# Kernel optimization log

Measured on AMD Instinct MI355X. Metric: run time of the kernel, lower is better.

The kernel has to match this reference:

```python
import jax, jax.numpy as jnp
import numpy as np

N = 50000
E = 800000
D_IN, D_HID, D_OUT = 128, 128, 64


def setup_inputs() -> dict:
    key = jax.random.key(0)
    ks = jax.random.split(key, 8)
    x = jax.random.normal(ks[0], (N, D_IN), dtype=jnp.float32)
    edge_index = jax.random.randint(ks[1], (2, E), 0, N, dtype=jnp.int64)
    # Glorot-ish init for GCNConv linear weights + zero bias (PyG default bias=True)
    def lin(k, din, dout):
        s = 1.0 / np.sqrt(din)
        return jax.random.uniform(k, (din, dout), jnp.float32, -s, s)
    return {
        "x": x,
        "edge_index": edge_index,
        "W1": lin(ks[2], D_IN, D_HID), "b1": jnp.zeros((D_HID,), jnp.float32),
        "W2": lin(ks[3], D_HID, D_HID), "b2": jnp.zeros((D_HID,), jnp.float32),
        "W3": lin(ks[4], D_HID, D_OUT), "b3": jnp.zeros((D_OUT,), jnp.float32),
    }


def _prep_edges(edge_index, n):
    # add self loops (PyG GCNConv default add_self_loops=True)
    loop = jnp.arange(n, dtype=edge_index.dtype)
    src = jnp.concatenate([edge_index[0], loop])
    dst = jnp.concatenate([edge_index[1], loop])
    deg = jax.ops.segment_sum(jnp.ones_like(dst, dtype=jnp.float32), dst, num_segments=n)
    dinv = jnp.where(deg > 0, jax.lax.rsqrt(deg), 0.0)
    norm = dinv[src] * dinv[dst]  # symmetric normalization per edge
    return src, dst, norm


def _gcn_conv(h, W, b, src, dst, norm, n):
    h = h @ W                                   # [N, dout]
    msg = h[src] * norm[:, None]                # [E+N, dout] gather
    out = jax.ops.segment_sum(msg, dst, num_segments=n)  # scatter-add
    return out + b


def reference(x, edge_index, W1, b1, W2, b2, W3, b3):
    src, dst, norm = _prep_edges(edge_index, N)
    h = jax.nn.relu(_gcn_conv(x, W1, b1, src, dst, norm, N))
    h = jax.nn.relu(_gcn_conv(h, W2, b2, src, dst, norm, N))
    return _gcn_conv(h, W3, b3, src, dst, norm, N)  # eval mode: dropout is identity
```

## Files before the change

kernel.cpp:

```cpp
#include <hip/hip_runtime.h>
#include <hip/hip_fp16.h>
#include <math.h>

#define NN 50000
#define NE 800000
#define RSTRIDE 104
#define RAWSTRIDE 96
#define NBUCK 196
#define BCAP 4608
#define ACH 4096

using bf8v = __attribute__((ext_vector_type(8))) short;
using f4v  = __attribute__((ext_vector_type(4))) float;

__device__ inline unsigned short f2bf(float f) {
    unsigned int u = __float_as_uint(f);
    u += 0x7FFFu + ((u >> 16) & 1u);
    return (unsigned short)(u >> 16);
}
__device__ inline float bflo(unsigned int d) { return __uint_as_float(d << 16); }
__device__ inline float bfhi(unsigned int d) { return __uint_as_float(d & 0xFFFF0000u); }
__device__ inline float ew(unsigned int u) {
    return __half2float(__ushort_as_half((unsigned short)(u >> 16)));
}
__device__ inline unsigned int epack(int col, float w) {
    return (unsigned int)col | ((unsigned int)__half_as_ushort(__float2half(w)) << 16);
}


__global__ __launch_bounds__(256) void bin_kernel(const int* __restrict__ src,
                                                  const int* __restrict__ dst,
                                                  int* __restrict__ gcursor,
                                                  unsigned int* __restrict__ bst) {
    __shared__ unsigned int items[ACH];
    __shared__ int cnt[256], pref[257], gstart[256];
    const int t = threadIdx.x;
    cnt[t] = 0;
    __syncthreads();
    const int base = blockIdx.x * ACH;

    unsigned int my[16]; int myb[16], myr[16];
    #pragma unroll
    for (int i = 0; i < 16; ++i) {
        int e = base + i * 256 + t;
        my[i] = 0; myb[i] = -1; myr[i] = 0;
        if (e < NE) {
            int d = dst[e], s = src[e];
            my[i] = (unsigned int)s | ((unsigned int)d << 16);
            int b = d >> 8;
            myb[i] = b;
            myr[i] = atomicAdd(&cnt[b], 1);
        }
    }
    __syncthreads();
    if (t == 0) {
        int run = 0;
        for (int b = 0; b < 256; ++b) { pref[b] = run; run += cnt[b]; }
        pref[256] = run;
    }
    __syncthreads();
    if (cnt[t] > 0) gstart[t] = atomicAdd(&gcursor[t], cnt[t]);
    __syncthreads();
    #pragma unroll
    for (int i = 0; i < 16; ++i)
        if (myb[i] >= 0) items[pref[myb[i]] + myr[i]] = my[i];
    __syncthreads();
    const int total = pref[256];
    for (int i = t; i < total; i += 256) {
        int lo = 0, hi = 255;
        while (lo < hi) { int mid = (lo + hi + 1) >> 1; if (pref[mid] <= i) lo = mid; else hi = mid - 1; }
        int idx = gstart[lo] + (i - pref[lo]);
        if (idx < BCAP) bst[(size_t)lo * BCAP + idx] = items[i];
    }
}


__global__ __launch_bounds__(512) void sortb_kernel(const int* __restrict__ gcursor,
                                                    const unsigned int* __restrict__ bst,
                                                    int* __restrict__ cnt_g,
                                                    unsigned short* __restrict__ raw) {
    __shared__ unsigned int items[BCAP];
    __shared__ int cnt[256], pref[257], cur[256];
    __shared__ unsigned short outl[BCAP];
    const int b = blockIdx.x;
    const int t = threadIdx.x;
    int n = gcursor[b];
    if (n > BCAP) n = BCAP;
    if (t < 256) { cnt[t] = 0; cur[t] = 0; }
    __syncthreads();
    for (int i = t; i < n; i += 512) {
        unsigned int u = bst[(size_t)b * BCAP + i];
        items[i] = u;
        atomicAdd(&cnt[(u >> 16) & 255], 1);
    }
    __syncthreads();
    if (t == 0) {
        int run = 0;
        for (int j = 0; j < 256; ++j) { pref[j] = run; run += cnt[j]; }
        pref[256] = run;
    }
    __syncthreads();
    for (int i = t; i < n; i += 512) {
        unsigned int u = items[i];
        int ln = (u >> 16) & 255;
        int r = atomicAdd(&cur[ln], 1);
        outl[pref[ln] + r] = (unsigned short)(u & 0xFFFFu);
    }
    __syncthreads();
    for (int i = t; i < n; i += 512) {
        int lo = 0, hi = 255;
        while (lo < hi) { int mid = (lo + hi + 1) >> 1; if (pref[mid] <= i) lo = mid; else hi = mid - 1; }
        int r = i - pref[lo];
        if (r < RAWSTRIDE) raw[(size_t)(b * 256 + lo) * RAWSTRIDE + r] = outl[i];
    }
    if (t < 256) {
        int node = b * 256 + t;
        if (node < NN) cnt_g[node] = cnt[t];
    }
}

__global__ __launch_bounds__(256) void dinv_kernel(const int* __restrict__ cnt_g,
                                                   float* __restrict__ dinv) {
    int i = blockIdx.x * 256 + threadIdx.x;
    if (i < NN) dinv[i] = rsqrtf((float)(1 + cnt_g[i]));
}

__global__ __launch_bounds__(256) void finalize_kernel(const int* __restrict__ cnt_g,
                                                       const unsigned short* __restrict__ raw,
                                                       const float* __restrict__ dinv,
                                                       unsigned int* __restrict__ eg,
                                                       int* __restrict__ degp) {
    int i = blockIdx.x * 256 + threadIdx.x;
    if (i >= NN) return;
    int c = cnt_g[i];
    if (c > RAWSTRIDE) c = RAWSTRIDE;
    int deg = 1 + c;
    float di = dinv[i];
    unsigned int* row = eg + (size_t)i * RSTRIDE;
    const unsigned short* rrow = raw + (size_t)i * RAWSTRIDE;
    row[0] = epack(i, di * di);
    int p = 1;
    for (int r = 0; r < c; ++r) {
        int col = rrow[r];
        row[p++] = epack(col, di * dinv[col]);
    }
    int dp = (deg + 7) & ~7;
    for (; p < dp; ++p) row[p] = 0u;
    degp[i] = dp;
}


template <bool A_FP32>
__global__ __launch_bounds__(256) void mfma_gemm_kernel(const void* __restrict__ Ain,
                                                        const float* __restrict__ W,
                                                        unsigned short* __restrict__ out) {
    __shared__ unsigned short Wt[128 * 136];
    __shared__ unsigned short Dt[64 * 136];
    const int t = threadIdx.x;
    const int row0 = blockIdx.x * 64;

    {
        int n = t & 127;
        int kbase = (t >> 7) * 4;
        for (int kk = kbase; kk < 128; kk += 8) {
            float w0 = W[(kk + 0) * 128 + n];
            float w1 = W[(kk + 1) * 128 + n];
            float w2 = W[(kk + 2) * 128 + n];
            float w3 = W[(kk + 3) * 128 + n];
            unsigned int p0 = (unsigned int)f2bf(w0) | ((unsigned int)f2bf(w1) << 16);
            unsigned int p1 = (unsigned int)f2bf(w2) | ((unsigned int)f2bf(w3) << 16);
            *(unsigned int*)&Wt[n * 136 + kk]     = p0;
            *(unsigned int*)&Wt[n * 136 + kk + 2] = p1;
        }
    }
    __syncthreads();

    const int wave = t >> 6;
    const int lane = t & 63;
    const int m16  = lane & 15;
    const int quad = lane >> 4;
    const int arow = row0 + wave * 16 + m16;
    const int arowc = (arow < NN) ? arow : 0;

    f4v acc[8];
    #pragma unroll
    for (int i = 0; i < 8; ++i) acc[i] = (f4v)(0.0f);

    #pragma unroll
    for (int k0 = 0; k0 < 128; k0 += 32) {
        bf8v afrag;
        if (A_FP32) {
            const float* A = (const float*)Ain;
            const float4* ap = (const float4*)(A + (size_t)arowc * 128 + k0 + quad * 8);
            float4 a0 = ap[0], a1 = ap[1];
            afrag[0] = (short)f2bf(a0.x); afrag[1] = (short)f2bf(a0.y);
            afrag[2] = (short)f2bf(a0.z); afrag[3] = (short)f2bf(a0.w);
            afrag[4] = (short)f2bf(a1.x); afrag[5] = (short)f2bf(a1.y);
            afrag[6] = (short)f2bf(a1.z); afrag[7] = (short)f2bf(a1.w);
        } else {
            const unsigned short* A = (const unsigned short*)Ain;
            afrag = *(const bf8v*)(A + (size_t)arowc * 128 + k0 + quad * 8);
        }
        #pragma unroll
        for (int nt = 0; nt < 8; ++nt) {
            bf8v bfrag = *(const bf8v*)&Wt[(nt * 16 + m16) * 136 + k0 + quad * 8];
            acc[nt] = __builtin_amdgcn_mfma_f32_16x16x32_bf16(afrag, bfrag, acc[nt], 0, 0, 0);
        }
    }

    #pragma unroll
    for (int nt = 0; nt < 8; ++nt) {
        #pragma unroll
        for (int r = 0; r < 4; ++r) {
            Dt[(wave * 16 + quad * 4 + r) * 136 + nt * 16 + m16] = f2bf(acc[nt][r]);
        }
    }
    __syncthreads();

    {
        int r = t >> 2;
        int c = t & 3;
        int gr = row0 + r;
        if (gr < NN) {
            const uint4* s = (const uint4*)&Dt[r * 136] + c * 4;
            uint4* d = (uint4*)(out + (size_t)gr * 128) + c * 4;
            d[0] = s[0]; d[1] = s[1]; d[2] = s[2]; d[3] = s[3];
        }
    }
}


template <bool RELU>
__global__ __launch_bounds__(256) void agg_bf16_kernel(const unsigned short* __restrict__ hin,
                                                       const unsigned int* __restrict__ eg,
                                                       const int* __restrict__ degp,
                                                       const float* __restrict__ bias,
                                                       unsigned short* __restrict__ outb) {
    const int t = threadIdx.x;
    const int group = t >> 4;
    const int lane  = t & 15;
    const int wid = blockIdx.x * 16 + group;
    if (wid >= NN) return;

    const int dp = degp[wid];
    const unsigned int* row = eg + (size_t)wid * RSTRIDE;
    const uint4* hv = (const uint4*)hin;

    float acc[8] = {0.f, 0.f, 0.f, 0.f, 0.f, 0.f, 0.f, 0.f};

    for (int e = 0; e < dp; e += 8) {
        uint4 q0 = ((const uint4*)(row + e))[0];
        uint4 q1 = ((const uint4*)(row + e))[1];
        uint4 g0 = hv[(size_t)(q0.x & 0xFFFFu) * 16 + lane];
        uint4 g1 = hv[(size_t)(q0.y & 0xFFFFu) * 16 + lane];
        uint4 g2 = hv[(size_t)(q0.z & 0xFFFFu) * 16 + lane];
        uint4 g3 = hv[(size_t)(q0.w & 0xFFFFu) * 16 + lane];
        uint4 g4 = hv[(size_t)(q1.x & 0xFFFFu) * 16 + lane];
        uint4 g5 = hv[(size_t)(q1.y & 0xFFFFu) * 16 + lane];
        uint4 g6 = hv[(size_t)(q1.z & 0xFFFFu) * 16 + lane];
        uint4 g7 = hv[(size_t)(q1.w & 0xFFFFu) * 16 + lane];
        float w0 = ew(q0.x), w1 = ew(q0.y), w2 = ew(q0.z), w3 = ew(q0.w);
        float w4 = ew(q1.x), w5 = ew(q1.y), w6 = ew(q1.z), w7 = ew(q1.w);
        #define ACCUM(G, W_) \
            acc[0] += W_ * bflo(G.x); acc[1] += W_ * bfhi(G.x); \
            acc[2] += W_ * bflo(G.y); acc[3] += W_ * bfhi(G.y); \
            acc[4] += W_ * bflo(G.z); acc[5] += W_ * bfhi(G.z); \
            acc[6] += W_ * bflo(G.w); acc[7] += W_ * bfhi(G.w);
        ACCUM(g0, w0) ACCUM(g1, w1) ACCUM(g2, w2) ACCUM(g3, w3)
        ACCUM(g4, w4) ACCUM(g5, w5) ACCUM(g6, w6) ACCUM(g7, w7)
        #undef ACCUM
    }

    const float4* bp = (const float4*)bias;
    float4 b0 = bp[lane * 2], b1 = bp[lane * 2 + 1];
    acc[0] += b0.x; acc[1] += b0.y; acc[2] += b0.z; acc[3] += b0.w;
    acc[4] += b1.x; acc[5] += b1.y; acc[6] += b1.z; acc[7] += b1.w;
    if (RELU) {
        #pragma unroll
        for (int j = 0; j < 8; ++j) acc[j] = fmaxf(acc[j], 0.f);
    }
    uint4 o;
    o.x = (unsigned int)f2bf(acc[0]) | ((unsigned int)f2bf(acc[1]) << 16);
    o.y = (unsigned int)f2bf(acc[2]) | ((unsigned int)f2bf(acc[3]) << 16);
    o.z = (unsigned int)f2bf(acc[4]) | ((unsigned int)f2bf(acc[5]) << 16);
    o.w = (unsigned int)f2bf(acc[6]) | ((unsigned int)f2bf(acc[7]) << 16);
    ((uint4*)(outb + (size_t)wid * 128))[lane] = o;
}


__global__ __launch_bounds__(256) void gemm3_kernel(const unsigned short* __restrict__ Ab,
                                                    const float* __restrict__ W,
                                                    unsigned short* __restrict__ outh) {
    constexpr int CG = 16;
    constexpr int RPT = 4;
    constexpr int ROWS = 64;
    constexpr int LD = 132;
    __shared__ float lds[ROWS * LD];
    const int t = threadIdx.x;
    const int row0 = blockIdx.x * ROWS;

    #pragma unroll
    for (int j = 0; j < ROWS / 8; ++j) {
        int idx4 = j * 256 + t;
        int r = idx4 >> 5, c4 = idx4 & 31;
        int gr = row0 + r;
        uint2 u = make_uint2(0u, 0u);
        if (gr < NN) u = ((const uint2*)(Ab + (size_t)gr * 128))[c4];
        float4 v;
        v.x = bflo(u.x); v.y = bfhi(u.x); v.z = bflo(u.y); v.w = bfhi(u.y);
        ((float4*)(lds + r * LD))[c4] = v;
    }
    __syncthreads();

    const int cg = t % CG;
    const int rt = t / CG;
    const float4* Wv = (const float4*)W;
    float4 acc[RPT];
    #pragma unroll
    for (int i = 0; i < RPT; ++i) acc[i] = make_float4(0.f, 0.f, 0.f, 0.f);

    for (int k0 = 0; k0 < 128; k0 += 4) {
        float4 w0 = Wv[(k0 + 0) * CG + cg];
        float4 w1 = Wv[(k0 + 1) * CG + cg];
        float4 w2 = Wv[(k0 + 2) * CG + cg];
        float4 w3 = Wv[(k0 + 3) * CG + cg];
        #pragma unroll
        for (int i = 0; i < RPT; ++i) {
            const float* lr = lds + (rt * RPT + i) * LD;
            float4 a = ((const float4*)lr)[k0 >> 2];
            acc[i].x += a.x * w0.x + a.y * w1.x + a.z * w2.x + a.w * w3.x;
            acc[i].y += a.x * w0.y + a.y * w1.y + a.z * w2.y + a.w * w3.y;
            acc[i].z += a.x * w0.z + a.y * w1.z + a.z * w2.z + a.w * w3.z;
            acc[i].w += a.x * w0.w + a.y * w1.w + a.z * w2.w + a.w * w3.w;
        }
    }

    #pragma unroll
    for (int i = 0; i < RPT; ++i) {
        int gr = row0 + rt * RPT + i;
        if (gr < NN) {
            uint2 o;
            o.x = (unsigned int)f2bf(acc[i].x) | ((unsigned int)f2bf(acc[i].y) << 16);
            o.y = (unsigned int)f2bf(acc[i].z) | ((unsigned int)f2bf(acc[i].w) << 16);
            ((uint2*)(outh + (size_t)gr * 64))[cg] = o;
        }
    }
}


__global__ __launch_bounds__(256) void agg3_kernel(const unsigned short* __restrict__ hin,
                                                   const unsigned int* __restrict__ eg,
                                                   const int* __restrict__ degp,
                                                   const float* __restrict__ bias,
                                                   float* __restrict__ out) {
    const int t = threadIdx.x;
    const int group = t >> 3;
    const int lane  = t & 7;
    const int wid = blockIdx.x * 32 + group;
    if (wid >= NN) return;

    const int dp = degp[wid];
    const unsigned int* row = eg + (size_t)wid * RSTRIDE;
    const uint4* hv = (const uint4*)hin;

    float acc[8] = {0.f, 0.f, 0.f, 0.f, 0.f, 0.f, 0.f, 0.f};

    for (int e = 0; e < dp; e += 8) {
        uint4 q0 = ((const uint4*)(row + e))[0];
        uint4 q1 = ((const uint4*)(row + e))[1];
        uint4 g0 = hv[(size_t)(q0.x & 0xFFFFu) * 8 + lane];
        uint4 g1 = hv[(size_t)(q0.y & 0xFFFFu) * 8 + lane];
        uint4 g2 = hv[(size_t)(q0.z & 0xFFFFu) * 8 + lane];
        uint4 g3 = hv[(size_t)(q0.w & 0xFFFFu) * 8 + lane];
        uint4 g4 = hv[(size_t)(q1.x & 0xFFFFu) * 8 + lane];
        uint4 g5 = hv[(size_t)(q1.y & 0xFFFFu) * 8 + lane];
        uint4 g6 = hv[(size_t)(q1.z & 0xFFFFu) * 8 + lane];
        uint4 g7 = hv[(size_t)(q1.w & 0xFFFFu) * 8 + lane];
        float w0 = ew(q0.x), w1 = ew(q0.y), w2 = ew(q0.z), w3 = ew(q0.w);
        float w4 = ew(q1.x), w5 = ew(q1.y), w6 = ew(q1.z), w7 = ew(q1.w);
        #define ACCUM(G, W_) \
            acc[0] += W_ * bflo(G.x); acc[1] += W_ * bfhi(G.x); \
            acc[2] += W_ * bflo(G.y); acc[3] += W_ * bfhi(G.y); \
            acc[4] += W_ * bflo(G.z); acc[5] += W_ * bfhi(G.z); \
            acc[6] += W_ * bflo(G.w); acc[7] += W_ * bfhi(G.w);
        ACCUM(g0, w0) ACCUM(g1, w1) ACCUM(g2, w2) ACCUM(g3, w3)
        ACCUM(g4, w4) ACCUM(g5, w5) ACCUM(g6, w6) ACCUM(g7, w7)
        #undef ACCUM
    }

    const float4* bp = (const float4*)bias;
    float4 b0 = bp[lane * 2], b1 = bp[lane * 2 + 1];
    acc[0] += b0.x; acc[1] += b0.y; acc[2] += b0.z; acc[3] += b0.w;
    acc[4] += b1.x; acc[5] += b1.y; acc[6] += b1.z; acc[7] += b1.w;

    float4 o0 = make_float4(acc[0], acc[1], acc[2], acc[3]);
    float4 o1 = make_float4(acc[4], acc[5], acc[6], acc[7]);
    ((float4*)(out + (size_t)wid * 64))[lane * 2]     = o0;
    ((float4*)(out + (size_t)wid * 64))[lane * 2 + 1] = o1;
}


extern "C" void kernel_launch(void* const* d_in, const int* in_sizes, int n_in,
                              void* d_out, int out_size, void* d_ws, size_t ws_size,
                              hipStream_t stream) {
    const float* x  = (const float*)d_in[0];
    const int*   ei = (const int*)d_in[1];
    const float* W1 = (const float*)d_in[2];
    const float* b1 = (const float*)d_in[3];
    const float* W2 = (const float*)d_in[4];
    const float* b2 = (const float*)d_in[5];
    const float* W3 = (const float*)d_in[6];
    const float* b3 = (const float*)d_in[7];
    float* out = (float*)d_out;

    char* w = (char*)d_ws;
    int*   cnt_g   = (int*)  (w + 0x0000000);
    int*   gcursor = (int*)  (w + 0x0040000);
    float* dinv    = (float*)(w + 0x0048000);
    int*   degp    = (int*)  (w + 0x0080000);
    unsigned int*   eg  = (unsigned int*)  (w + 0x0140000);
    unsigned int*   bst = (unsigned int*)  (w + 0x1540000);
    unsigned short* hb  = (unsigned short*)(w + 0x1A00000);
    unsigned short* zb  = (unsigned short*)(w + 0x2680000);
    unsigned short* raw = (unsigned short*)(w + 0x2680000);
    unsigned short* h3b = (unsigned short*)(w + 0x3300000);

    const int* src = ei;
    const int* dst = ei + NE;

    hipMemsetAsync(gcursor, 0, NBUCK * sizeof(int), stream);
    bin_kernel<<<(NE + ACH - 1) / ACH, 256, 0, stream>>>(src, dst, gcursor, bst);
    sortb_kernel<<<NBUCK, 512, 0, stream>>>(gcursor, bst, cnt_g, raw);
    dinv_kernel<<<(NN + 255) / 256, 256, 0, stream>>>(cnt_g, dinv);
    finalize_kernel<<<(NN + 255) / 256, 256, 0, stream>>>(cnt_g, raw, dinv, eg, degp);

    mfma_gemm_kernel<true><<<(NN + 63) / 64, 256, 0, stream>>>(x, W1, hb);
    agg_bf16_kernel<true><<<(NN + 15) / 16, 256, 0, stream>>>(hb, eg, degp, b1, zb);
    mfma_gemm_kernel<false><<<(NN + 63) / 64, 256, 0, stream>>>(zb, W2, hb);
    agg_bf16_kernel<true><<<(NN + 15) / 16, 256, 0, stream>>>(hb, eg, degp, b2, zb);
    gemm3_kernel<<<(NN + 63) / 64, 256, 0, stream>>>(zb, W3, h3b);
    agg3_kernel<<<(NN + 31) / 32, 256, 0, stream>>>(h3b, eg, degp, b3, out);
}
```

Before: 268.5 us.

## Drop packed edge list; aggregate directly from 16-bit CSR with on-the-fly weights

Removes the dinv and finalize kernels by computing degree, inverse sqrt-degree and padded row length inside the bucket sort kernel, padding rows with a sentinel index. The aggregation kernels now read 16-bit column indices straight from the raw CSR, handle the self loop separately, and compute edge weights as dinv[dst]*dinv[src] through an extra gather per edge. This saves two launches and the write and read of the packed 32-bit edge array, at the cost of extra random dinv loads and select logic in the three aggregation passes.

```diff
diff --git a/kernel.cpp b/kernel.cpp
--- a/kernel.cpp
+++ b/kernel.cpp
@@ -1,10 +1,8 @@
 #include <hip/hip_runtime.h>
-#include <hip/hip_fp16.h>
 #include <math.h>
 
 #define NN 50000
 #define NE 800000
-#define RSTRIDE 104
 #define RAWSTRIDE 96
 #define NBUCK 196
 #define BCAP 4608
@@ -20,12 +18,6 @@
 }
 __device__ inline float bflo(unsigned int d) { return __uint_as_float(d << 16); }
 __device__ inline float bfhi(unsigned int d) { return __uint_as_float(d & 0xFFFF0000u); }
-__device__ inline float ew(unsigned int u) {
-    return __half2float(__ushort_as_half((unsigned short)(u >> 16)));
-}
-__device__ inline unsigned int epack(int col, float w) {
-    return (unsigned int)col | ((unsigned int)__half_as_ushort(__float2half(w)) << 16);
-}
 
 
 __global__ __launch_bounds__(256) void bin_kernel(const int* __restrict__ src,
@@ -77,7 +69,8 @@
 
 __global__ __launch_bounds__(512) void sortb_kernel(const int* __restrict__ gcursor,
                                                     const unsigned int* __restrict__ bst,
-                                                    int* __restrict__ cnt_g,
+                                                    float* __restrict__ dinv,
+                                                    int* __restrict__ degp,
                                                     unsigned short* __restrict__ raw) {
     __shared__ unsigned int items[BCAP];
     __shared__ int cnt[256], pref[257], cur[256];
@@ -115,38 +108,16 @@
     }
     if (t < 256) {
         int node = b * 256 + t;
-        if (node < NN) cnt_g[node] = cnt[t];
-    }
-}
-
-__global__ __launch_bounds__(256) void dinv_kernel(const int* __restrict__ cnt_g,
-                                                   float* __restrict__ dinv) {
-    int i = blockIdx.x * 256 + threadIdx.x;
-    if (i < NN) dinv[i] = rsqrtf((float)(1 + cnt_g[i]));
-}
-
-__global__ __launch_bounds__(256) void finalize_kernel(const int* __restrict__ cnt_g,
-                                                       const unsigned short* __restrict__ raw,
-                                                       const float* __restrict__ dinv,
-                                                       unsigned int* __restrict__ eg,
-                                                       int* __restrict__ degp) {
-    int i = blockIdx.x * 256 + threadIdx.x;
-    if (i >= NN) return;
-    int c = cnt_g[i];
-    if (c > RAWSTRIDE) c = RAWSTRIDE;
-    int deg = 1 + c;
-    float di = dinv[i];
-    unsigned int* row = eg + (size_t)i * RSTRIDE;
-    const unsigned short* rrow = raw + (size_t)i * RAWSTRIDE;
-    row[0] = epack(i, di * di);
-    int p = 1;
-    for (int r = 0; r < c; ++r) {
-        int col = rrow[r];
-        row[p++] = epack(col, di * dinv[col]);
-    }
-    int dp = (deg + 7) & ~7;
-    for (; p < dp; ++p) row[p] = 0u;
-    degp[i] = dp;
+        if (node < NN) {
+            int c = cnt[t];
+            int cc = (c > RAWSTRIDE) ? RAWSTRIDE : c;
+            int dp = (cc + 7) & ~7;
+            degp[node] = dp;
+            dinv[node] = rsqrtf((float)(1 + c));
+            for (int r = cc; r < dp; ++r)
+                raw[(size_t)node * RAWSTRIDE + r] = 0xFFFFu;
+        }
+    }
 }
 
 
@@ -232,8 +203,9 @@
 
 template <bool RELU>
 __global__ __launch_bounds__(256) void agg_bf16_kernel(const unsigned short* __restrict__ hin,
-                                                       const unsigned int* __restrict__ eg,
+                                                       const unsigned short* __restrict__ raw,
                                                        const int* __restrict__ degp,
+                                                       const float* __restrict__ dinv,
                                                        const float* __restrict__ bias,
                                                        unsigned short* __restrict__ outb) {
     const int t = threadIdx.x;
@@ -243,32 +215,52 @@
     if (wid >= NN) return;
 
     const int dp = degp[wid];
-    const unsigned int* row = eg + (size_t)wid * RSTRIDE;
+    const float di = dinv[wid];
+    const unsigned short* row = raw + (size_t)wid * RAWSTRIDE;
     const uint4* hv = (const uint4*)hin;
 
     float acc[8] = {0.f, 0.f, 0.f, 0.f, 0.f, 0.f, 0.f, 0.f};
 
+    #define ACCUM(G, W_) \
+        acc[0] += W_ * bflo(G.x); acc[1] += W_ * bfhi(G.x); \
+        acc[2] += W_ * bflo(G.y); acc[3] += W_ * bfhi(G.y); \
+        acc[4] += W_ * bflo(G.z); acc[5] += W_ * bfhi(G.z); \
+        acc[6] += W_ * bflo(G.w); acc[7] += W_ * bfhi(G.w);
+
+    {
+        uint4 gs = hv[(size_t)wid * 16 + lane];
+        float ws = di * di;
+        ACCUM(gs, ws)
+    }
+
     for (int e = 0; e < dp; e += 8) {
-        uint4 q0 = ((const uint4*)(row + e))[0];
-        uint4 q1 = ((const uint4*)(row + e))[1];
-        uint4 g0 = hv[(size_t)(q0.x & 0xFFFFu) * 16 + lane];
-        uint4 g1 = hv[(size_t)(q0.y & 0xFFFFu) * 16 + lane];
-        uint4 g2 = hv[(size_t)(q0.z & 0xFFFFu) * 16 + lane];
-        uint4 g3 = hv[(size_t)(q0.w & 0xFFFFu) * 16 + lane];
-        uint4 g4 = hv[(size_t)(q1.x & 0xFFFFu) * 16 + lane];
-        uint4 g5 = hv[(size_t)(q1.y & 0xFFFFu) * 16 + lane];
-        uint4 g6 = hv[(size_t)(q1.z & 0xFFFFu) * 16 + lane];
-        uint4 g7 = hv[(size_t)(q1.w & 0xFFFFu) * 16 + lane];
-        float w0 = ew(q0.x), w1 = ew(q0.y), w2 = ew(q0.z), w3 = ew(q0.w);
-        float w4 = ew(q1.x), w5 = ew(q1.y), w6 = ew(q1.z), w7 = ew(q1.w);
-        #define ACCUM(G, W_) \
-            acc[0] += W_ * bflo(G.x); acc[1] += W_ * bfhi(G.x); \
-            acc[2] += W_ * bflo(G.y); acc[3] += W_ * bfhi(G.y); \
-            acc[4] += W_ * bflo(G.z); acc[5] += W_ * bfhi(G.z); \
-            acc[6] += W_ * bflo(G.w); acc[7] += W_ * bfhi(G.w);
+        uint4 q = *(const uint4*)(row + e);
+        int c0 = q.x & 0xFFFF, c1 = q.x >> 16;
+        int c2 = q.y & 0xFFFF, c3 = q.y >> 16;
+        int c4 = q.z & 0xFFFF, c5 = q.z >> 16;
+        int c6 = q.w & 0xFFFF, c7 = q.w >> 16;
+        int k0 = (c0 < NN) ? c0 : 0, k1 = (c1 < NN) ? c1 : 0;
+        int k2 = (c2 < NN) ? c2 : 0, k3 = (c3 < NN) ? c3 : 0;
+        int k4 = (c4 < NN) ? c4 : 0, k5 = (c5 < NN) ? c5 : 0;
+        int k6 = (c6 < NN) ? c6 : 0, k7 = (c7 < NN) ? c7 : 0;
+        float w0 = (c0 < NN) ? di * dinv[k0] : 0.f;
+        float w1 = (c1 < NN) ? di * dinv[k1] : 0.f;
+        float w2 = (c2 < NN) ? di * dinv[k2] : 0.f;
+        float w3 = (c3 < NN) ? di * dinv[k3] : 0.f;
+        float w4 = (c4 < NN) ? di * dinv[k4] : 0.f;
+        float w5 = (c5 < NN) ? di * dinv[k5] : 0.f;
+        float w6 = (c6 < NN) ? di * dinv[k6] : 0.f;
+        float w7 = (c7 < NN) ? di * dinv[k7] : 0.f;
+        uint4 g0 = hv[(size_t)k0 * 16 + lane];
+        uint4 g1 = hv[(size_t)k1 * 16 + lane];
+        uint4 g2 = hv[(size_t)k2 * 16 + lane];
+        uint4 g3 = hv[(size_t)k3 * 16 + lane];
+        uint4 g4 = hv[(size_t)k4 * 16 + lane];
+        uint4 g5 = hv[(size_t)k5 * 16 + lane];
+        uint4 g6 = hv[(size_t)k6 * 16 + lane];
+        uint4 g7 = hv[(size_t)k7 * 16 + lane];
         ACCUM(g0, w0) ACCUM(g1, w1) ACCUM(g2, w2) ACCUM(g3, w3)
         ACCUM(g4, w4) ACCUM(g5, w5) ACCUM(g6, w6) ACCUM(g7, w7)
-        #undef ACCUM
     }
 
     const float4* bp = (const float4*)bias;
@@ -285,6 +277,7 @@
     o.z = (unsigned int)f2bf(acc[4]) | ((unsigned int)f2bf(acc[5]) << 16);
     o.w = (unsigned int)f2bf(acc[6]) | ((unsigned int)f2bf(acc[7]) << 16);
     ((uint4*)(outb + (size_t)wid * 128))[lane] = o;
+    #undef ACCUM
 }
 
 
@@ -349,8 +342,9 @@
 
 
 __global__ __launch_bounds__(256) void agg3_kernel(const unsigned short* __restrict__ hin,
-                                                   const unsigned int* __restrict__ eg,
+                                                   const unsigned short* __restrict__ raw,
                                                    const int* __restrict__ degp,
+                                                   const float* __restrict__ dinv,
                                                    const float* __restrict__ bias,
                                                    float* __restrict__ out) {
     const int t = threadIdx.x;
@@ -360,33 +354,54 @@
     if (wid >= NN) return;
 
     const int dp = degp[wid];
-    const unsigned int* row = eg + (size_t)wid * RSTRIDE;
+    const float di = dinv[wid];
+    const unsigned short* row = raw + (size_t)wid * RAWSTRIDE;
     const uint4* hv = (const uint4*)hin;
 
     float acc[8] = {0.f, 0.f, 0.f, 0.f, 0.f, 0.f, 0.f, 0.f};
 
+    #define ACCUM(G, W_) \
+        acc[0] += W_ * bflo(G.x); acc[1] += W_ * bfhi(G.x); \
+        acc[2] += W_ * bflo(G.y); acc[3] += W_ * bfhi(G.y); \
+        acc[4] += W_ * bflo(G.z); acc[5] += W_ * bfhi(G.z); \
+        acc[6] += W_ * bflo(G.w); acc[7] += W_ * bfhi(G.w);
+
+    {
+        uint4 gs = hv[(size_t)wid * 8 + lane];
+        float ws = di * di;
+        ACCUM(gs, ws)
+    }
+
     for (int e = 0; e < dp; e += 8) {
-        uint4 q0 = ((const uint4*)(row + e))[0];
-        uint4 q1 = ((const uint4*)(row + e))[1];
-        uint4 g0 = hv[(size_t)(q0.x & 0xFFFFu) * 8 + lane];
-        uint4 g1 = hv[(size_t)(q0.y & 0xFFFFu) * 8 + lane];
-        uint4 g2 = hv[(size_t)(q0.z & 0xFFFFu) * 8 + lane];
-        uint4 g3 = hv[(size_t)(q0.w & 0xFFFFu) * 8 + lane];
-        uint4 g4 = hv[(size_t)(q1.x & 0xFFFFu) * 8 + lane];
-        uint4 g5 = hv[(size_t)(q1.y & 0xFFFFu) * 8 + lane];
-        uint4 g6 = hv[(size_t)(q1.z & 0xFFFFu) * 8 + lane];
-        uint4 g7 = hv[(size_t)(q1.w & 0xFFFFu) * 8 + lane];
-        float w0 = ew(q0.x), w1 = ew(q0.y), w2 = ew(q0.z), w3 = ew(q0.w);
-        float w4 = ew(q1.x), w5 = ew(q1.y), w6 = ew(q1.z), w7 = ew(q1.w);
-        #define ACCUM(G, W_) \
-            acc[0] += W_ * bflo(G.x); acc[1] += W_ * bfhi(G.x); \
-            acc[2] += W_ * bflo(G.y); acc[3] += W_ * bfhi(G.y); \
-            acc[4] += W_ * bflo(G.z); acc[5] += W_ * bfhi(G.z); \
-            acc[6] += W_ * bflo(G.w); acc[7] += W_ * bfhi(G.w);
+        uint4 q = *(const uint4*)(row + e);
+        int c0 = q.x & 0xFFFF, c1 = q.x >> 16;
+        int c2 = q.y & 0xFFFF, c3 = q.y >> 16;
+        int c4 = q.z & 0xFFFF, c5 = q.z >> 16;
+        int c6 = q.w & 0xFFFF, c7 = q.w >> 16;
+        int k0 = (c0 < NN) ? c0 : 0, k1 = (c1 < NN) ? c1 : 0;
+        int k2 = (c2 < NN) ? c2 : 0, k3 = (c3 < NN) ? c3 : 0;
+        int k4 = (c4 < NN) ? c4 : 0, k5 = (c5 < NN) ? c5 : 0;
+        int k6 = (c6 < NN) ? c6 : 0, k7 = (c7 < NN) ? c7 : 0;
+        float w0 = (c0 < NN) ? di * dinv[k0] : 0.f;
+        float w1 = (c1 < NN) ? di * dinv[k1] : 0.f;
+        float w2 = (c2 < NN) ? di * dinv[k2] : 0.f;
+        float w3 = (c3 < NN) ? di * dinv[k3] : 0.f;
+        float w4 = (c4 < NN) ? di * dinv[k4] : 0.f;
+        float w5 = (c5 < NN) ? di * dinv[k5] : 0.f;
+        float w6 = (c6 < NN) ? di * dinv[k6] : 0.f;
+        float w7 = (c7 < NN) ? di * dinv[k7] : 0.f;
+        uint4 g0 = hv[(size_t)k0 * 8 + lane];
+        uint4 g1 = hv[(size_t)k1 * 8 + lane];
+        uint4 g2 = hv[(size_t)k2 * 8 + lane];
+        uint4 g3 = hv[(size_t)k3 * 8 + lane];
+        uint4 g4 = hv[(size_t)k4 * 8 + lane];
+        uint4 g5 = hv[(size_t)k5 * 8 + lane];
+        uint4 g6 = hv[(size_t)k6 * 8 + lane];
+        uint4 g7 = hv[(size_t)k7 * 8 + lane];
         ACCUM(g0, w0) ACCUM(g1, w1) ACCUM(g2, w2) ACCUM(g3, w3)
         ACCUM(g4, w4) ACCUM(g5, w5) ACCUM(g6, w6) ACCUM(g7, w7)
-        #undef ACCUM
-    }
+    }
+    #undef ACCUM
 
     const float4* bp = (const float4*)bias;
     float4 b0 = bp[lane * 2], b1 = bp[lane * 2 + 1];
@@ -414,30 +429,26 @@
     float* out = (float*)d_out;
 
     char* w = (char*)d_ws;
-    int*   cnt_g   = (int*)  (w + 0x0000000);
     int*   gcursor = (int*)  (w + 0x0040000);
     float* dinv    = (float*)(w + 0x0048000);
     int*   degp    = (int*)  (w + 0x0080000);
-    unsigned int*   eg  = (unsigned int*)  (w + 0x0140000);
-    unsigned int*   bst = (unsigned int*)  (w + 0x1540000);
-    unsigned short* hb  = (unsigned short*)(w + 0x1A00000);
-    unsigned short* zb  = (unsigned short*)(w + 0x2680000);
-    unsigned short* raw = (unsigned short*)(w + 0x2680000);
-    unsigned short* h3b = (unsigned short*)(w + 0x3300000);
+    unsigned int*   bst = (unsigned int*)  (w + 0x0140000);
+    unsigned short* raw = (unsigned short*)(w + 0x0500000);
+    unsigned short* hb  = (unsigned short*)(w + 0x1000000);
+    unsigned short* zb  = (unsigned short*)(w + 0x1D00000);
+    unsigned short* h3b = (unsigned short*)(w + 0x2A00000);
 
     const int* src = ei;
     const int* dst = ei + NE;
 
     hipMemsetAsync(gcursor, 0, NBUCK * sizeof(int), stream);
     bin_kernel<<<(NE + ACH - 1) / ACH, 256, 0, stream>>>(src, dst, gcursor, bst);
-    sortb_kernel<<<NBUCK, 512, 0, stream>>>(gcursor, bst, cnt_g, raw);
-    dinv_kernel<<<(NN + 255) / 256, 256, 0, stream>>>(cnt_g, dinv);
-    finalize_kernel<<<(NN + 255) / 256, 256, 0, stream>>>(cnt_g, raw, dinv, eg, degp);
+    sortb_kernel<<<NBUCK, 512, 0, stream>>>(gcursor, bst, dinv, degp, raw);
 
     mfma_gemm_kernel<true><<<(NN + 63) / 64, 256, 0, stream>>>(x, W1, hb);
-    agg_bf16_kernel<true><<<(NN + 15) / 16, 256, 0, stream>>>(hb, eg, degp, b1, zb);
+    agg_bf16_kernel<true><<<(NN + 15) / 16, 256, 0, stream>>>(hb, raw, degp, dinv, b1, zb);
     mfma_gemm_kernel<false><<<(NN + 63) / 64, 256, 0, stream>>>(zb, W2, hb);
-    agg_bf16_kernel<true><<<(NN + 15) / 16, 256, 0, stream>>>(hb, eg, degp, b2, zb);
+    agg_bf16_kernel<true><<<(NN + 15) / 16, 256, 0, stream>>>(hb, raw, degp, dinv, b2, zb);
     gemm3_kernel<<<(NN + 63) / 64, 256, 0, stream>>>(zb, W3, h3b);
-    agg3_kernel<<<(NN + 31) / 32, 256, 0, stream>>>(h3b, eg, degp, b3, out);
-}
+    agg3_kernel<<<(NN + 31) / 32, 256, 0, stream>>>(h3b, raw, degp, dinv, b3, out);
+}
```

New measurement: 274.8 us. +2.4%, slower.
